# Optimization experiments

Measured on AMD Instinct MI355X. Metric: run time of the kernel, lower is better.

Reference implementation:

```python
import jax, jax.numpy as jnp
import numpy as np

N = 8192      # nodes (N_features)
D = 64        # oscillator dimension
E_K = 262144  # Kuramoto coupling edges
E_HK = 262144 # Hopfield-Kuramoto coupling edges
H = 64        # interaction MLP hidden width (N_weights)
KAPPA_K = 2.0
KAPPA_H = 2.0


def setup_inputs() -> dict:
    key = jax.random.key(0)
    ks = jax.random.split(key, 9)
    return dict(
        state_H=jax.random.normal(ks[0], (N,), dtype=jnp.float32),
        state_K=jax.random.normal(ks[1], (N, D), dtype=jnp.float32),
        W_H=jax.random.normal(ks[2], (N, N), dtype=jnp.float32) / np.float32(np.sqrt(N)),
        omega=jax.random.normal(ks[3], (D, D), dtype=jnp.float32),
        w1=jax.random.normal(ks[4], (1, H), dtype=jnp.float32),
        b1=jnp.zeros((H,), dtype=jnp.float32),
        w2=jax.random.normal(ks[5], (H, 1), dtype=jnp.float32) / np.float32(np.sqrt(H)),
        ind_K=jax.random.randint(ks[6], (E_K, 2), 0, N),
        ind_HK=jax.random.randint(ks[7], (E_HK, 2), 0, N),
    )


def _interaction_K(s, w1, b1, w2):
    # edgewise scalar MLP: [E] -> [E], dE/ds of the Kuramoto interaction energy
    h = jnp.tanh(s[:, None] @ w1 + b1)  # [E, H]
    return (h @ w2)[:, 0]               # [E]


def reference(state_H, state_K, W_H, omega, w1, b1, w2, ind_K, ind_HK):
    # normalize oscillator states onto unit sphere (per node)
    state_K = state_K / jnp.linalg.norm(state_K, axis=1, keepdims=True)

    i, j = ind_HK[:, 0], ind_HK[:, 1]
    Gram = jnp.sum(state_K[i] * state_K[j], axis=1)  # [E_HK]

    # Hopfield model: g = LNet.get_g(state_H), f_H = Hopfield_model(t, state_H, ...)
    g = jnp.tanh(state_H)                 # [N]
    f_H = -state_H + W_H @ g              # [N] dense Hopfield dynamics
    f_H = f_H.at[i].add(Gram * g[j] / KAPPA_H)
    f_H = f_H.at[j].add(Gram * g[i] / KAPPA_H)

    # Kuramoto edge coupling
    p, q = ind_K[:, 0], ind_K[:, 1]
    s = jnp.sum(state_K[p] * state_K[q], axis=1)        # [E_K]
    dE_ds = _interaction_K(s, w1, b1, w2)[:, None]      # [E_K, 1]
    f_K = jnp.zeros_like(state_K)
    f_K = f_K.at[p].add(dE_ds * state_K[q])
    f_K = f_K.at[q].add(dE_ds * state_K[p])

    # Hopfield->Kuramoto coupling
    G = (g[i] * g[j])[:, None]                          # [E_HK, 1]
    f_K = f_K.at[i].add(-G * state_K[j] / KAPPA_K)
    f_K = f_K.at[j].add(-G * state_K[i] / KAPPA_K)

    # project onto tangent of the sphere + antisymmetric rotation
    f_K = (-f_K
           + state_K * jnp.sum(state_K * f_K, axis=1, keepdims=True)
           + state_K @ ((omega - omega.T) * 0.5))
    return (f_H, f_K)
```

## Files before the change

kernel.cpp:

```cpp
#include <hip/hip_runtime.h>
#include <math.h>

#define N 8192
#define D 64
#define E_K 262144
#define E_HK 262144
#define NEDGE (E_K + E_HK)
#define CAP 256

constexpr float INV_KAPPA = 0.5f;

__device__ inline float fast_tanh(float x) {
  x = fminf(15.f, fmaxf(-15.f, x));
  float e = __expf(2.f * x);
  return (e - 1.f) * __builtin_amdgcn_rcpf(e + 1.f);
}

__device__ inline float wave_reduce(float v) {
  #pragma unroll
  for (int off = 32; off > 0; off >>= 1) v += __shfl_xor(v, off);
  return v;
}

__global__ __launch_bounds__(256) void prep_kernel(
    const float* __restrict__ state_K, const float* __restrict__ state_H,
    const float* __restrict__ omega,
    float* __restrict__ Knorm, float* __restrict__ g, float* __restrict__ Om) {
  int tid  = blockIdx.x * blockDim.x + threadIdx.x;
  int wave = tid >> 6;
  int lane = threadIdx.x & 63;
  if (wave < N) {
    float v = state_K[wave * D + lane];
    float ss = wave_reduce(v * v);
    Knorm[wave * D + lane] = v * __builtin_amdgcn_rcpf(sqrtf(ss));
  }
  if (tid < N) g[tid] = fast_tanh(state_H[tid]);
  if (tid < D * D) {
    int a = tid >> 6, b = tid & 63;
    Om[tid] = 0.5f * (omega[a * D + b] - omega[b * D + a]);
  }
}

__global__ __launch_bounds__(256) void scatter_kernel(
    const int* __restrict__ ind_HK, const int* __restrict__ ind_K,
    int* __restrict__ cursor, int* __restrict__ entries) {
  int t = blockIdx.x * blockDim.x + threadIdx.x;
  if (t >= NEDGE) return;
  int i, j, bit;
  if (t < E_HK) {
    int2 e = ((const int2*)ind_HK)[t];
    i = e.x; j = e.y; bit = (int)0x80000000;
  } else {
    int2 e = ((const int2*)ind_K)[t - E_HK];
    i = e.x; j = e.y; bit = 0;
  }
  int s0 = atomicAdd(&cursor[i], 1);
  if (s0 < CAP) entries[i * CAP + s0] = j | bit;
  int s1 = atomicAdd(&cursor[j], 1);
  if (s1 < CAP) entries[j * CAP + s1] = i | bit;
}

__global__ __launch_bounds__(256) void matvec_kernel(
    const float* __restrict__ W_H, const float* __restrict__ g,
    const float* __restrict__ state_H, float* __restrict__ f_H) {
  int row = blockIdx.x;
  const float4* Wrow = reinterpret_cast<const float4*>(W_H + (size_t)row * N);
  const float4* g4   = reinterpret_cast<const float4*>(g);
  float acc = 0.0f;
  #pragma unroll
  for (int c = threadIdx.x; c < N / 4; c += 256) {
    float4 w = Wrow[c];
    float4 gg = g4[c];
    acc += w.x * gg.x + w.y * gg.y + w.z * gg.z + w.w * gg.w;
  }
  acc = wave_reduce(acc);
  __shared__ float sbuf[4];
  if ((threadIdx.x & 63) == 0) sbuf[threadIdx.x >> 6] = acc;
  __syncthreads();
  if (threadIdx.x == 0)
    f_H[row] = -state_H[row] + sbuf[0] + sbuf[1] + sbuf[2] + sbuf[3];
}

__global__ __launch_bounds__(256) void gather_kernel(
    const float* __restrict__ Knorm, const float* __restrict__ g,
    const float* __restrict__ Om, const float* __restrict__ w1,
    const float* __restrict__ b1, const float* __restrict__ w2,
    const int* __restrict__ cursor, const int* __restrict__ entries,
    float* __restrict__ f_H, float* __restrict__ f_K) {
  __shared__ int   sh_ent[CAP];
  __shared__ float sAcc[4][D];
  __shared__ float sH[4];
  int row  = blockIdx.x;
  int lane = threadIdx.x & 63;
  int wv   = threadIdx.x >> 6;
  int len  = min(cursor[row], CAP);
  for (int e = threadIdx.x; e < len; e += 256)
    sh_ent[e] = entries[row * CAP + e];
  float kr  = Knorm[row * D + lane];
  float gr  = g[row];
  float w1l = w1[lane], b1l = b1[lane], w2l = w2[lane];
  __syncthreads();
  float acc  = 0.f;
  float sumH = 0.f;
  for (int e = wv; e < len; e += 4) {
    int ent   = sh_ent[e];
    int other = ent & 0x7FFFFFFF;
    float ko  = Knorm[other * D + lane];
    float dot = wave_reduce(kr * ko);
    if (ent < 0) {
      float go = g[other];
      acc  += (-gr * go * INV_KAPPA) * ko;
      sumH += dot * go * INV_KAPPA;
    } else {
      float de = wave_reduce(fast_tanh(dot * w1l + b1l) * w2l);
      acc += de * ko;
    }
  }
  sAcc[wv][lane] = acc;
  if (lane == 0) sH[wv] = sumH;
  __syncthreads();
  if (wv == 0) {
    float tot = sAcc[0][lane] + sAcc[1][lane] + sAcc[2][lane] + sAcc[3][lane];
    float rd = wave_reduce(kr * tot);
    float ko = 0.f;
    #pragma unroll
    for (int d = 0; d < D; ++d)
      ko += __shfl(kr, d) * Om[d * D + lane];
    f_K[row * D + lane] = -tot + kr * rd + ko;
    if (lane == 0) f_H[row] += sH[0] + sH[1] + sH[2] + sH[3];
  }
}

extern "C" void kernel_launch(void* const* d_in, const int* in_sizes, int n_in,
                              void* d_out, int out_size, void* d_ws, size_t ws_size,
                              hipStream_t stream) {
  const float* state_H = (const float*)d_in[0];
  const float* state_K = (const float*)d_in[1];
  const float* W_H     = (const float*)d_in[2];
  const float* omega   = (const float*)d_in[3];
  const float* w1      = (const float*)d_in[4];
  const float* b1      = (const float*)d_in[5];
  const float* w2      = (const float*)d_in[6];
  const int*   ind_K   = (const int*)d_in[7];
  const int*   ind_HK  = (const int*)d_in[8];

  float* f_H = (float*)d_out;
  float* f_K = (float*)d_out + N;

  char* ws = (char*)d_ws;
  int*   entries = (int*)ws;                ws += (size_t)N * CAP * sizeof(int);
  float* Knorm   = (float*)ws;              ws += (size_t)N * D * sizeof(float);
  float* g       = (float*)ws;              ws += N * sizeof(float);
  float* Om      = (float*)ws;              ws += D * D * sizeof(float);
  int*   cursor  = (int*)ws;

  hipMemsetAsync(cursor, 0, N * sizeof(int), stream);
  prep_kernel<<<(N * 64) / 256, 256, 0, stream>>>(state_K, state_H, omega,
                                                  Knorm, g, Om);
  scatter_kernel<<<NEDGE / 256, 256, 0, stream>>>(ind_HK, ind_K, cursor, entries);
  matvec_kernel<<<N, 256, 0, stream>>>(W_H, g, state_H, f_H);
  gather_kernel<<<N, 256, 0, stream>>>(Knorm, g, Om, w1, b1, w2,
                                       cursor, entries, f_H, f_K);
}
```

Baseline: 544.2 us.

## Fuse prep with scatter and matvec with gather into two kernels

Merges the prep and edge-scatter kernels into one launch, with block ranges doing different jobs. Merges the dense W_H matvec into the per-row gather kernel: W rows are prefetched into registers up front, so that HBM traffic overlaps the irregular neighbour gathers. For Hopfield edges it accumulates g*ko per lane and does a single dot at the end, replacing a wave reduction per edge. The cost is higher register pressure from the 8 float4 held per thread, which may lower occupancy.

```diff
diff --git a/kernel.cpp b/kernel.cpp
--- a/kernel.cpp
+++ b/kernel.cpp
@@ -22,112 +22,116 @@
   return v;
 }
 
-__global__ __launch_bounds__(256) void prep_kernel(
+__global__ __launch_bounds__(256) void prep_scatter_kernel(
     const float* __restrict__ state_K, const float* __restrict__ state_H,
     const float* __restrict__ omega,
-    float* __restrict__ Knorm, float* __restrict__ g, float* __restrict__ Om) {
-  int tid  = blockIdx.x * blockDim.x + threadIdx.x;
-  int wave = tid >> 6;
-  int lane = threadIdx.x & 63;
-  if (wave < N) {
-    float v = state_K[wave * D + lane];
+    const int* __restrict__ ind_HK, const int* __restrict__ ind_K,
+    float* __restrict__ Knorm, float* __restrict__ g, float* __restrict__ Om,
+    int* __restrict__ cursor, int* __restrict__ entries) {
+  int b = blockIdx.x;
+  if (b < 2048) {
+    int t = b * 256 + threadIdx.x;
+    int i, j, bit;
+    if (t < E_HK) {
+      int2 e = ((const int2*)ind_HK)[t];
+      i = e.x; j = e.y; bit = (int)0x80000000;
+    } else {
+      int2 e = ((const int2*)ind_K)[t - E_HK];
+      i = e.x; j = e.y; bit = 0;
+    }
+    int s0 = atomicAdd(&cursor[i], 1);
+    if (s0 < CAP) entries[i * CAP + s0] = j | bit;
+    int s1 = atomicAdd(&cursor[j], 1);
+    if (s1 < CAP) entries[j * CAP + s1] = i | bit;
+  } else if (b < 4096) {
+    int lane = threadIdx.x & 63;
+    int row  = (b - 2048) * 4 + (threadIdx.x >> 6);
+    float v  = state_K[row * D + lane];
     float ss = wave_reduce(v * v);
-    Knorm[wave * D + lane] = v * __builtin_amdgcn_rcpf(sqrtf(ss));
-  }
-  if (tid < N) g[tid] = fast_tanh(state_H[tid]);
-  if (tid < D * D) {
-    int a = tid >> 6, b = tid & 63;
-    Om[tid] = 0.5f * (omega[a * D + b] - omega[b * D + a]);
+    Knorm[row * D + lane] = v * __builtin_amdgcn_rcpf(sqrtf(ss));
+    if (lane == 0) g[row] = fast_tanh(state_H[row]);
+  } else {
+    for (int t = threadIdx.x; t < D * D; t += 256) {
+      int a = t >> 6, c = t & 63;
+      Om[t] = 0.5f * (omega[a * D + c] - omega[c * D + a]);
+    }
   }
 }
 
-__global__ __launch_bounds__(256) void scatter_kernel(
-    const int* __restrict__ ind_HK, const int* __restrict__ ind_K,
-    int* __restrict__ cursor, int* __restrict__ entries) {
-  int t = blockIdx.x * blockDim.x + threadIdx.x;
-  if (t >= NEDGE) return;
-  int i, j, bit;
-  if (t < E_HK) {
-    int2 e = ((const int2*)ind_HK)[t];
-    i = e.x; j = e.y; bit = (int)0x80000000;
-  } else {
-    int2 e = ((const int2*)ind_K)[t - E_HK];
-    i = e.x; j = e.y; bit = 0;
-  }
-  int s0 = atomicAdd(&cursor[i], 1);
-  if (s0 < CAP) entries[i * CAP + s0] = j | bit;
-  int s1 = atomicAdd(&cursor[j], 1);
-  if (s1 < CAP) entries[j * CAP + s1] = i | bit;
-}
-
-__global__ __launch_bounds__(256) void matvec_kernel(
-    const float* __restrict__ W_H, const float* __restrict__ g,
-    const float* __restrict__ state_H, float* __restrict__ f_H) {
-  int row = blockIdx.x;
-  const float4* Wrow = reinterpret_cast<const float4*>(W_H + (size_t)row * N);
-  const float4* g4   = reinterpret_cast<const float4*>(g);
-  float acc = 0.0f;
-  #pragma unroll
-  for (int c = threadIdx.x; c < N / 4; c += 256) {
-    float4 w = Wrow[c];
-    float4 gg = g4[c];
-    acc += w.x * gg.x + w.y * gg.y + w.z * gg.z + w.w * gg.w;
-  }
-  acc = wave_reduce(acc);
-  __shared__ float sbuf[4];
-  if ((threadIdx.x & 63) == 0) sbuf[threadIdx.x >> 6] = acc;
-  __syncthreads();
-  if (threadIdx.x == 0)
-    f_H[row] = -state_H[row] + sbuf[0] + sbuf[1] + sbuf[2] + sbuf[3];
-}
-
-__global__ __launch_bounds__(256) void gather_kernel(
+__global__ __launch_bounds__(256) void mega_kernel(
+    const float* __restrict__ W_H, const float* __restrict__ state_H,
     const float* __restrict__ Knorm, const float* __restrict__ g,
     const float* __restrict__ Om, const float* __restrict__ w1,
     const float* __restrict__ b1, const float* __restrict__ w2,
     const int* __restrict__ cursor, const int* __restrict__ entries,
     float* __restrict__ f_H, float* __restrict__ f_K) {
-  __shared__ int   sh_ent[CAP];
-  __shared__ float sAcc[4][D];
-  __shared__ float sH[4];
   int row  = blockIdx.x;
   int lane = threadIdx.x & 63;
   int wv   = threadIdx.x >> 6;
-  int len  = min(cursor[row], CAP);
-  for (int e = threadIdx.x; e < len; e += 256)
-    sh_ent[e] = entries[row * CAP + e];
+
+  const float4* Wrow = reinterpret_cast<const float4*>(W_H + (size_t)row * N);
+  float4 wreg[8];
+  #pragma unroll
+  for (int k = 0; k < 8; ++k) wreg[k] = Wrow[threadIdx.x + k * 256];
+
   float kr  = Knorm[row * D + lane];
   float gr  = g[row];
   float w1l = w1[lane], b1l = b1[lane], w2l = w2[lane];
+
+  __shared__ int sh_ent[CAP];
+  int len = min(cursor[row], CAP);
+  for (int e = threadIdx.x; e < len; e += 256)
+    sh_ent[e] = entries[row * CAP + e];
   __syncthreads();
+
   float acc  = 0.f;
-  float sumH = 0.f;
+  float accH = 0.f;
   for (int e = wv; e < len; e += 4) {
     int ent   = sh_ent[e];
     int other = ent & 0x7FFFFFFF;
     float ko  = Knorm[other * D + lane];
-    float dot = wave_reduce(kr * ko);
     if (ent < 0) {
       float go = g[other];
       acc  += (-gr * go * INV_KAPPA) * ko;
-      sumH += dot * go * INV_KAPPA;
+      accH += go * ko;
     } else {
-      float de = wave_reduce(fast_tanh(dot * w1l + b1l) * w2l);
+      float dot = wave_reduce(kr * ko);
+      float de  = wave_reduce(fast_tanh(dot * w1l + b1l) * w2l);
       acc += de * ko;
     }
   }
-  sAcc[wv][lane] = acc;
-  if (lane == 0) sH[wv] = sumH;
+
+  const float4* g4 = reinterpret_cast<const float4*>(g);
+  float mv = 0.f;
+  #pragma unroll
+  for (int k = 0; k < 8; ++k) {
+    float4 gg = g4[threadIdx.x + k * 256];
+    mv += wreg[k].x * gg.x + wreg[k].y * gg.y +
+          wreg[k].z * gg.z + wreg[k].w * gg.w;
+  }
+  mv = wave_reduce(mv);
+
+  __shared__ float sAcc[4][D];
+  __shared__ float sAccH[4][D];
+  __shared__ float sMv[4];
+  sAcc[wv][lane]  = acc;
+  sAccH[wv][lane] = accH;
+  if (lane == 0) sMv[wv] = mv;
   __syncthreads();
+
   if (wv == 0) {
-    float tot = sAcc[0][lane] + sAcc[1][lane] + sAcc[2][lane] + sAcc[3][lane];
+    float tot  = sAcc[0][lane] + sAcc[1][lane] + sAcc[2][lane] + sAcc[3][lane];
+    float totH = sAccH[0][lane] + sAccH[1][lane] + sAccH[2][lane] + sAccH[3][lane];
     float rd = wave_reduce(kr * tot);
-    float ko = 0.f;
+    float sh = wave_reduce(kr * totH);
+    float krot = 0.f;
     #pragma unroll
     for (int d = 0; d < D; ++d)
-      ko += __shfl(kr, d) * Om[d * D + lane];
-    f_K[row * D + lane] = -tot + kr * rd + ko;
-    if (lane == 0) f_H[row] += sH[0] + sH[1] + sH[2] + sH[3];
+      krot += __shfl(kr, d) * Om[d * D + lane];
+    f_K[row * D + lane] = -tot + kr * rd + krot;
+    if (lane == 0)
+      f_H[row] = -state_H[row] + sMv[0] + sMv[1] + sMv[2] + sMv[3]
+                 + sh * INV_KAPPA;
   }
 }
 
@@ -148,17 +152,15 @@
   float* f_K = (float*)d_out + N;
 
   char* ws = (char*)d_ws;
-  int*   entries = (int*)ws;                ws += (size_t)N * CAP * sizeof(int);
-  float* Knorm   = (float*)ws;              ws += (size_t)N * D * sizeof(float);
-  float* g       = (float*)ws;              ws += N * sizeof(float);
-  float* Om      = (float*)ws;              ws += D * D * sizeof(float);
+  int*   entries = (int*)ws;               ws += (size_t)N * CAP * sizeof(int);
+  float* Knorm   = (float*)ws;             ws += (size_t)N * D * sizeof(float);
+  float* g       = (float*)ws;             ws += N * sizeof(float);
+  float* Om      = (float*)ws;             ws += D * D * sizeof(float);
   int*   cursor  = (int*)ws;
 
   hipMemsetAsync(cursor, 0, N * sizeof(int), stream);
-  prep_kernel<<<(N * 64) / 256, 256, 0, stream>>>(state_K, state_H, omega,
-                                                  Knorm, g, Om);
-  scatter_kernel<<<NEDGE / 256, 256, 0, stream>>>(ind_HK, ind_K, cursor, entries);
-  matvec_kernel<<<N, 256, 0, stream>>>(W_H, g, state_H, f_H);
-  gather_kernel<<<N, 256, 0, stream>>>(Knorm, g, Om, w1, b1, w2,
-                                       cursor, entries, f_H, f_K);
+  prep_scatter_kernel<<<4097, 256, 0, stream>>>(
+      state_K, state_H, omega, ind_HK, ind_K, Knorm, g, Om, cursor, entries);
+  mega_kernel<<<N, 256, 0, stream>>>(W_H, state_H, Knorm, g, Om, w1, b1, w2,
+                                     cursor, entries, f_H, f_K);
 }
```

Result: faster. 499.2 us (-8.3%).
